# Kernel tuning notes

Hardware: AMD Instinct MI355X
Metric: run time of the kernel (lower is better)

Reference implementation:

```python
import jax, jax.numpy as jnp
import numpy as np

N_NODES, IN_FEAT, N_HEADS, N_HIDDEN = 4096, 1433, 8, 64
NEG_SLOPE = 0.2

def setup_inputs() -> dict:
    key = jax.random.key(0)
    k1, k2, k3 = jax.random.split(key, 3)
    vertex = jax.random.normal(k1, (N_NODES, IN_FEAT), dtype=jnp.float32)
    # linear_vert: Linear(in_features, n_hidden*n_heads, bias=False) -> weight [H*d, F]
    W_vert = jax.random.normal(k2, (N_HEADS * N_HIDDEN, IN_FEAT), dtype=jnp.float32) * (1.0 / np.sqrt(IN_FEAT))
    # attn: Linear(n_heads, n_heads, bias=False) -> weight [H, H]
    W_attn = jax.random.normal(k3, (N_HEADS, N_HEADS), dtype=jnp.float32) * (1.0 / np.sqrt(N_HEADS))
    return {"vertex": vertex, "W_vert": W_vert, "W_attn": W_attn}

def reference(vertex, W_vert, W_attn):
    n = vertex.shape[0]
    # g_vertex: [N, H, d]
    g = (vertex @ W_vert.T).reshape(n, N_HEADS, N_HIDDEN)
    # per-head Gram matrices, stacked on last dim: [N, N, H]
    gram = jnp.einsum('nhd,mhd->nmh', g, g)
    # head-mixing linear (H->H) + leaky relu, then sum over heads: [N, N]
    e = jax.nn.leaky_relu(jnp.einsum('nmh,gh->nmg', gram, W_attn), negative_slope=NEG_SLOPE)
    return e.sum(axis=-1)
```

## Files before the change

### kernel.cpp

```cpp
#include <hip/hip_runtime.h>
#include <hip/hip_bf16.h>

#define NN   4096
#define FIN  1433
#define KPAD 1536
#define NH   8
#define ND   64
#define CD   512

typedef float f32x4 __attribute__((ext_vector_type(4)));
typedef short s16x8 __attribute__((ext_vector_type(8)));

#define MFMA16(a, b, c) __builtin_amdgcn_mfma_f32_16x16x32_bf16((a), (b), (c), 0, 0, 0)

__device__ __forceinline__ void gload_lds16(const void* g, void* l) {
  __builtin_amdgcn_global_load_lds((const __attribute__((address_space(1))) void*)g,
                                   (__attribute__((address_space(3))) void*)l, 16, 0, 0);
}

__device__ __forceinline__ ushort f2bf(float x) {
  __hip_bfloat16 b = __float2bfloat16(x);
  ushort u;
  __builtin_memcpy(&u, &b, 2);
  return u;
}

__global__ void castpad_kernel(const float* __restrict__ src, ushort* __restrict__ dst,
                               int rows, int kin, int kout) {
  int i = blockIdx.x * blockDim.x + threadIdx.x;
  int kg = kout >> 3;
  int total = rows * kg;
  if (i >= total) return;
  int r  = i / kg;
  int k0 = (i - r * kg) << 3;
  s16x8 v;
#pragma unroll
  for (int j = 0; j < 8; ++j) {
    int k = k0 + j;
    float f = (k < kin) ? src[(size_t)r * kin + k] : 0.0f;
    v[j] = (short)f2bf(f);
  }
  *reinterpret_cast<s16x8*>(&dst[(size_t)r * kout + k0]) = v;
}

__global__ __launch_bounds__(256, 2) void gemm1_kernel(const ushort* __restrict__ A,
                                                       const ushort* __restrict__ B,
                                                       ushort* __restrict__ G) {
  __shared__ ushort As[2][64][128];
  __shared__ ushort Bs[2][64][128];
  const int tid  = threadIdx.x;
  const int lane = tid & 63;
  const int w    = tid >> 6;
  const int wr   = w >> 1, wc = w & 1;
  const int row0 = blockIdx.y * 64;
  const int col0 = blockIdx.x * 64;

  f32x4 acc[2][2] = {};

  auto stage = [&](int buf, int k0) {
#pragma unroll
    for (int j = 0; j < 4; ++j) {
      int ci = (w * 4 + j) * 64 + lane;
      int r  = ci >> 4;
      int cp = ci & 15;
      int gc = cp ^ (r & 7);
      gload_lds16(A + (size_t)(row0 + r) * KPAD + k0 + gc * 8,
                  &As[buf][0][0] + (size_t)(w * 4 + j) * 512);
      gload_lds16(B + (size_t)(col0 + r) * KPAD + k0 + gc * 8,
                  &Bs[buf][0][0] + (size_t)(w * 4 + j) * 512);
    }
  };

  stage(0, 0);
  __syncthreads();
  int cur = 0;

  for (int k0 = 0; k0 < KPAD; k0 += 128) {
    if (k0 + 128 < KPAD) stage(cur ^ 1, k0 + 128);
#pragma unroll
    for (int kk = 0; kk < 4; ++kk) {
      int kq = kk * 4 + (lane >> 4);
      s16x8 af[2], bfv[2];
#pragma unroll
      for (int f = 0; f < 2; ++f) {
        int ar = wr * 32 + f * 16 + (lane & 15);
        af[f]  = *reinterpret_cast<const s16x8*>(&As[cur][ar][(kq ^ (ar & 7)) * 8]);
        int br = wc * 32 + f * 16 + (lane & 15);
        bfv[f] = *reinterpret_cast<const s16x8*>(&Bs[cur][br][(kq ^ (br & 7)) * 8]);
      }
#pragma unroll
      for (int fi = 0; fi < 2; ++fi)
#pragma unroll
        for (int fj = 0; fj < 2; ++fj)
          acc[fi][fj] = MFMA16(af[fi], bfv[fj], acc[fi][fj]);
    }
    __syncthreads();
    cur ^= 1;
  }

#pragma unroll
  for (int fi = 0; fi < 2; ++fi)
#pragma unroll
    for (int fj = 0; fj < 2; ++fj)
#pragma unroll
      for (int r = 0; r < 4; ++r) {
        int gr = row0 + wr * 32 + fi * 16 + (lane >> 4) * 4 + r;
        int gcol = col0 + wc * 32 + fj * 16 + (lane & 15);
        G[(size_t)gr * CD + gcol] = f2bf(acc[fi][fj][r]);
      }
}

__global__ __launch_bounds__(256, 2) void gram_kernel(const ushort* __restrict__ G,
                                                      const float* __restrict__ Wattn,
                                                      float* __restrict__ out) {
  const int nwg = (NN / 64) * (NN / 64 + 1) / 2;
  const int cpx = nwg / 8;
  int b = blockIdx.x;
  int t = (b % 8) * cpx + (b / 8);
  int bi = (int)((129.0f - sqrtf(16641.0f - 8.0f * (float)t)) * 0.5f);
  while ((129 * (bi + 1) - (bi + 1) * (bi + 1)) / 2 <= t) ++bi;
  while ((129 * bi - bi * bi) / 2 > t) --bi;
  const int bj = bi + (t - (129 * bi - bi * bi) / 2);
  const int ri0 = bi * 64, ci0 = bj * 64;

  __shared__ union LdsU {
    struct { ushort A[64][256]; ushort B[64][256]; } s;
    float t[64][65];
  } lds;
  __shared__ float sW[8][8];

  const int tid  = threadIdx.x;
  const int lane = tid & 63;
  const int w    = tid >> 6;
  const int wr   = w >> 1, wc = w & 1;

  if (tid < 64) sW[tid >> 3][tid & 7] = Wattn[tid];

  f32x4 acc[8][2][2] = {};

  auto stage = [&](int p) {
#pragma unroll
    for (int j = 0; j < 8; ++j) {
      int ci = (w * 8 + j) * 64 + lane;
      int r  = ci >> 5;
      int cp = ci & 31;
      int gc = cp ^ (r & 7);
      gload_lds16(G + (size_t)(ri0 + r) * CD + p * 256 + gc * 8,
                  &lds.s.A[0][0] + (size_t)(w * 8 + j) * 512);
      gload_lds16(G + (size_t)(ci0 + r) * CD + p * 256 + gc * 8,
                  &lds.s.B[0][0] + (size_t)(w * 8 + j) * 512);
    }
  };

  auto compute = [&](int p) {
#pragma unroll
    for (int hh = 0; hh < 4; ++hh) {
#pragma unroll
      for (int kk = 0; kk < 2; ++kk) {
        int kq = kk * 4 + (lane >> 4);
        s16x8 af[2], bfv[2];
#pragma unroll
        for (int f = 0; f < 2; ++f) {
          int ar = wr * 32 + f * 16 + (lane & 15);
          af[f]  = *reinterpret_cast<const s16x8*>(
                     &lds.s.A[ar][((hh * 8 + kq) ^ (ar & 7)) * 8]);
          int br = wc * 32 + f * 16 + (lane & 15);
          bfv[f] = *reinterpret_cast<const s16x8*>(
                     &lds.s.B[br][((hh * 8 + kq) ^ (br & 7)) * 8]);
        }
        int h = p * 4 + hh;
#pragma unroll
        for (int fi = 0; fi < 2; ++fi)
#pragma unroll
          for (int fj = 0; fj < 2; ++fj)
            acc[h][fi][fj] = MFMA16(af[fi], bfv[fj], acc[h][fi][fj]);
      }
    }
  };

  stage(0);
  __syncthreads();
  compute(0);
  __syncthreads();
  stage(1);
  __syncthreads();
  compute(1);

  float o[2][2][4] = {};
#pragma unroll
  for (int g = 0; g < 8; ++g) {
    float z[2][2][4] = {};
#pragma unroll
    for (int h = 0; h < 8; ++h) {
      float wgh = sW[g][h];
#pragma unroll
      for (int fi = 0; fi < 2; ++fi)
#pragma unroll
        for (int fj = 0; fj < 2; ++fj)
#pragma unroll
          for (int r = 0; r < 4; ++r)
            z[fi][fj][r] = fmaf(acc[h][fi][fj][r], wgh, z[fi][fj][r]);
    }
#pragma unroll
    for (int fi = 0; fi < 2; ++fi)
#pragma unroll
      for (int fj = 0; fj < 2; ++fj)
#pragma unroll
        for (int r = 0; r < 4; ++r) {
          float zz = z[fi][fj][r];
          o[fi][fj][r] += fmaxf(zz, 0.2f * zz);
        }
  }

#pragma unroll
  for (int fi = 0; fi < 2; ++fi)
#pragma unroll
    for (int fj = 0; fj < 2; ++fj)
#pragma unroll
      for (int r = 0; r < 4; ++r) {
        int rr = wr * 32 + fi * 16 + (lane >> 4) * 4 + r;
        int cc = wc * 32 + fj * 16 + (lane & 15);
        out[(size_t)(ri0 + rr) * NN + ci0 + cc] = o[fi][fj][r];
      }

  if (bi != bj) {
    __syncthreads();
#pragma unroll
    for (int fi = 0; fi < 2; ++fi)
#pragma unroll
      for (int fj = 0; fj < 2; ++fj)
#pragma unroll
        for (int r = 0; r < 4; ++r) {
          int rr = wr * 32 + fi * 16 + (lane >> 4) * 4 + r;
          int cc = wc * 32 + fj * 16 + (lane & 15);
          lds.t[cc][rr] = o[fi][fj][r];
        }
    __syncthreads();
    int a  = tid >> 2;
    int cb = (tid & 3) * 16;
#pragma unroll
    for (int jj = 0; jj < 4; ++jj) {
      float4 v;
      v.x = lds.t[a][cb + jj * 4 + 0];
      v.y = lds.t[a][cb + jj * 4 + 1];
      v.z = lds.t[a][cb + jj * 4 + 2];
      v.w = lds.t[a][cb + jj * 4 + 3];
      *reinterpret_cast<float4*>(&out[(size_t)(ci0 + a) * NN + ri0 + cb + jj * 4]) = v;
    }
  }
}

extern "C" void kernel_launch(void* const* d_in, const int* in_sizes, int n_in,
                              void* d_out, int out_size, void* d_ws, size_t ws_size,
                              hipStream_t stream) {
  const float* vertex = (const float*)d_in[0];
  const float* Wvert  = (const float*)d_in[1];
  const float* Wattn  = (const float*)d_in[2];
  float* out = (float*)d_out;

  char* ws = (char*)d_ws;
  ushort* Va = (ushort*)ws;
  ushort* Wb = (ushort*)(ws + (size_t)NN * KPAD * 2);
  ushort* G  = (ushort*)(ws + (size_t)NN * KPAD * 2 + (size_t)CD * KPAD * 2);

  int tot1 = NN * (KPAD / 8);
  castpad_kernel<<<(tot1 + 255) / 256, 256, 0, stream>>>(vertex, Va, NN, FIN, KPAD);
  int tot2 = CD * (KPAD / 8);
  castpad_kernel<<<(tot2 + 255) / 256, 256, 0, stream>>>(Wvert, Wb, CD, FIN, KPAD);

  gemm1_kernel<<<dim3(CD / 64, NN / 64), 256, 0, stream>>>(Va, Wb, G);

  int ntri = (NN / 64) * (NN / 64 + 1) / 2;
  gram_kernel<<<ntri, 256, 0, stream>>>(G, Wattn, out);
}
```

Measured before the change: 193.1 us.

## Double-buffer gram K loop, stage output through LDS with nontemporal stores, remap gemm1 blocks

The gram kernel now splits the 512-wide feature dimension into four 128-wide stages held in double-buffered LDS, so the next stage's global loads overlap the current stage's MFMAs instead of running strictly one after the other. The direct output tile is also transposed through LDS and written as coalesced 16-byte nontemporal stores, matching the mirrored tile. The gemm1 launch becomes a 1D grid with a block remap so that blocks sharing A rows are grouped, for cache locality. These changes add barriers and an extra LDS round-trip for the direct tile.

```diff
diff --git a/kernel.cpp b/kernel.cpp
--- a/kernel.cpp
+++ b/kernel.cpp
@@ -52,8 +52,14 @@
   const int lane = tid & 63;
   const int w    = tid >> 6;
   const int wr   = w >> 1, wc = w & 1;
-  const int row0 = blockIdx.y * 64;
-  const int col0 = blockIdx.x * 64;
+
+  const int b    = blockIdx.x;
+  const int x    = b & 7;
+  const int slot = b >> 3;
+  const int by   = x * 8 + (slot >> 3);
+  const int bx   = slot & 7;
+  const int row0 = by * 64;
+  const int col0 = bx * 64;
 
   f32x4 acc[2][2] = {};
 
@@ -124,7 +130,7 @@
   const int ri0 = bi * 64, ci0 = bj * 64;
 
   __shared__ union LdsU {
-    struct { ushort A[64][256]; ushort B[64][256]; } s;
+    struct { ushort A[2][64][128]; ushort B[2][64][128]; } s;
     float t[64][65];
   } lds;
   __shared__ float sW[8][8];
@@ -138,37 +144,37 @@
 
   f32x4 acc[8][2][2] = {};
 
-  auto stage = [&](int p) {
-#pragma unroll
-    for (int j = 0; j < 8; ++j) {
-      int ci = (w * 8 + j) * 64 + lane;
-      int r  = ci >> 5;
-      int cp = ci & 31;
+  auto stage = [&](int buf, int s) {
+#pragma unroll
+    for (int j = 0; j < 4; ++j) {
+      int ci = (w * 4 + j) * 64 + lane;
+      int r  = ci >> 4;
+      int cp = ci & 15;
       int gc = cp ^ (r & 7);
-      gload_lds16(G + (size_t)(ri0 + r) * CD + p * 256 + gc * 8,
-                  &lds.s.A[0][0] + (size_t)(w * 8 + j) * 512);
-      gload_lds16(G + (size_t)(ci0 + r) * CD + p * 256 + gc * 8,
-                  &lds.s.B[0][0] + (size_t)(w * 8 + j) * 512);
+      gload_lds16(G + (size_t)(ri0 + r) * CD + s * 128 + gc * 8,
+                  &lds.s.A[buf][0][0] + (size_t)(w * 4 + j) * 512);
+      gload_lds16(G + (size_t)(ci0 + r) * CD + s * 128 + gc * 8,
+                  &lds.s.B[buf][0][0] + (size_t)(w * 4 + j) * 512);
     }
   };
 
-  auto compute = [&](int p) {
-#pragma unroll
-    for (int hh = 0; hh < 4; ++hh) {
+  auto compute = [&](int buf, int s) {
+#pragma unroll
+    for (int hh = 0; hh < 2; ++hh) {
 #pragma unroll
       for (int kk = 0; kk < 2; ++kk) {
-        int kq = kk * 4 + (lane >> 4);
+        int kq = hh * 8 + kk * 4 + (lane >> 4);
         s16x8 af[2], bfv[2];
 #pragma unroll
         for (int f = 0; f < 2; ++f) {
           int ar = wr * 32 + f * 16 + (lane & 15);
           af[f]  = *reinterpret_cast<const s16x8*>(
-                     &lds.s.A[ar][((hh * 8 + kq) ^ (ar & 7)) * 8]);
+                     &lds.s.A[buf][ar][(kq ^ (ar & 7)) * 8]);
           int br = wc * 32 + f * 16 + (lane & 15);
           bfv[f] = *reinterpret_cast<const s16x8*>(
-                     &lds.s.B[br][((hh * 8 + kq) ^ (br & 7)) * 8]);
+                     &lds.s.B[buf][br][(kq ^ (br & 7)) * 8]);
         }
-        int h = p * 4 + hh;
+        int h = s * 2 + hh;
 #pragma unroll
         for (int fi = 0; fi < 2; ++fi)
 #pragma unroll
@@ -178,13 +184,16 @@
     }
   };
 
-  stage(0);
-  __syncthreads();
-  compute(0);
-  __syncthreads();
-  stage(1);
-  __syncthreads();
-  compute(1);
+  stage(0, 0);
+  __syncthreads();
+  int cur = 0;
+#pragma unroll
+  for (int s = 0; s < 4; ++s) {
+    if (s < 3) stage(cur ^ 1, s + 1);
+    compute(cur, s);
+    __syncthreads();
+    cur ^= 1;
+  }
 
   float o[2][2][4] = {};
 #pragma unroll
@@ -212,6 +221,10 @@
         }
   }
 
+  const int a  = tid >> 2;
+  const int cb = (tid & 3) * 16;
+
+  __syncthreads();
 #pragma unroll
   for (int fi = 0; fi < 2; ++fi)
 #pragma unroll
@@ -220,8 +233,17 @@
       for (int r = 0; r < 4; ++r) {
         int rr = wr * 32 + fi * 16 + (lane >> 4) * 4 + r;
         int cc = wc * 32 + fj * 16 + (lane & 15);
-        out[(size_t)(ri0 + rr) * NN + ci0 + cc] = o[fi][fj][r];
-      }
+        lds.t[rr][cc] = o[fi][fj][r];
+      }
+  __syncthreads();
+#pragma unroll
+  for (int jj = 0; jj < 4; ++jj) {
+    f32x4 v;
+#pragma unroll
+    for (int e = 0; e < 4; ++e) v[e] = lds.t[a][cb + jj * 4 + e];
+    __builtin_nontemporal_store(
+        v, reinterpret_cast<f32x4*>(&out[(size_t)(ri0 + a) * NN + ci0 + cb + jj * 4]));
+  }
 
   if (bi != bj) {
     __syncthreads();
@@ -236,16 +258,13 @@
           lds.t[cc][rr] = o[fi][fj][r];
         }
     __syncthreads();
-    int a  = tid >> 2;
-    int cb = (tid & 3) * 16;
 #pragma unroll
     for (int jj = 0; jj < 4; ++jj) {
-      float4 v;
-      v.x = lds.t[a][cb + jj * 4 + 0];
-      v.y = lds.t[a][cb + jj * 4 + 1];
-      v.z = lds.t[a][cb + jj * 4 + 2];
-      v.w = lds.t[a][cb + jj * 4 + 3];
-      *reinterpret_cast<float4*>(&out[(size_t)(ci0 + a) * NN + ri0 + cb + jj * 4]) = v;
+      f32x4 v;
+#pragma unroll
+      for (int e = 0; e < 4; ++e) v[e] = lds.t[a][cb + jj * 4 + e];
+      __builtin_nontemporal_store(
+          v, reinterpret_cast<f32x4*>(&out[(size_t)(ci0 + a) * NN + ri0 + cb + jj * 4]));
     }
   }
 }
@@ -268,7 +287,7 @@
   int tot2 = CD * (KPAD / 8);
   castpad_kernel<<<(tot2 + 255) / 256, 256, 0, stream>>>(Wvert, Wb, CD, FIN, KPAD);
 
-  gemm1_kernel<<<dim3(CD / 64, NN / 64), 256, 0, stream>>>(Va, Wb, G);
+  gemm1_kernel<<<512, 256, 0, stream>>>(Va, Wb, G);
 
   int ntri = (NN / 64) * (NN / 64 + 1) / 2;
   gram_kernel<<<ntri, 256, 0, stream>>>(G, Wattn, out);
```

After: 245.0 us. 26.9% more time.
